# Optimization experiments

Measured on AMD Instinct MI355X. Metric: run time of the kernel, lower is better.

Reference implementation:

```python
import jax, jax.numpy as jnp
import numpy as np

LN_EPS = 1e-5
K = 3  # pointops.interpolation uses 3-NN

def _ln(x, g, b):
    mu = jnp.mean(x, axis=-1, keepdims=True)
    var = jnp.mean((x - mu) ** 2, axis=-1, keepdims=True)
    return (x - mu) * jax.lax.rsqrt(var + LN_EPS) * g + b

def setup_inputs() -> dict:
    key = jax.random.key(0)
    ks = jax.random.split(key, 8)
    B, n, m = 4, 4096, 16384        # coarse pts / fine pts per batch segment
    Cin, Cout = 384, 192
    feats = jax.random.normal(ks[0], (B * n, Cin), jnp.float32)
    xyz = jax.random.uniform(ks[1], (B * n, 3), jnp.float32)
    support_xyz = jax.random.uniform(ks[2], (B * m, 3), jnp.float32)
    support_feats = jax.random.normal(ks[3], (B * m, Cout), jnp.float32)
    offset = ((jnp.arange(B) + 1) * n).astype(jnp.int32)
    support_offset = ((jnp.arange(B) + 1) * m).astype(jnp.int32)
    # linear1: LayerNorm(Cout) -> Linear(Cout, Cout); linear2: LayerNorm(Cin) -> Linear(Cin, Cout)
    ln1_g = jnp.ones((Cout,), jnp.float32); ln1_b = jnp.zeros((Cout,), jnp.float32)
    w1 = jax.random.normal(ks[4], (Cout, Cout), jnp.float32) / np.sqrt(Cout)
    b1 = jnp.zeros((Cout,), jnp.float32)
    ln2_g = jnp.ones((Cin,), jnp.float32); ln2_b = jnp.zeros((Cin,), jnp.float32)
    w2 = jax.random.normal(ks[5], (Cin, Cout), jnp.float32) / np.sqrt(Cin)
    b2 = jnp.zeros((Cout,), jnp.float32)
    return {"feats": feats, "xyz": xyz, "support_xyz": support_xyz,
            "support_feats": support_feats, "offset": offset,
            "support_offset": support_offset, "ln1_g": ln1_g, "ln1_b": ln1_b,
            "w1": w1, "b1": b1, "ln2_g": ln2_g, "ln2_b": ln2_b, "w2": w2, "b2": b2}

def _interp_one(args):
    # src_xyz [n,3], dst_xyz [m,3], src_feat [n,C] -> [m,C]
    src_xyz, dst_xyz, src_feat = args
    d2 = jnp.sum((dst_xyz[:, None, :] - src_xyz[None, :, :]) ** 2, axis=-1)  # [m,n]
    neg_d2, idx = jax.lax.top_k(-d2, K)                                      # 3 nearest
    dist = jnp.sqrt(jnp.maximum(-neg_d2, 0.0))
    recip = 1.0 / (dist + 1e-8)
    w = recip / jnp.sum(recip, axis=-1, keepdims=True)                       # [m,K]
    return jnp.einsum('mk,mkc->mc', w, src_feat[idx])

def reference(feats, xyz, support_xyz, support_feats, offset, support_offset,
              ln1_g, ln1_b, w1, b1, ln2_g, ln2_b, w2, b2):
    B = offset.shape[0]
    n = feats.shape[0] // B
    m = support_feats.shape[0] // B
    # branch 2: LN+Linear on coarse feats, then 3-NN inverse-distance interpolation to fine points
    h = _ln(feats, ln2_g, ln2_b) @ w2 + b2                                   # [B*n, Cout]
    interp = jax.lax.map(_interp_one, (xyz.reshape(B, n, 3),
                                       support_xyz.reshape(B, m, 3),
                                       h.reshape(B, n, -1)))                 # [B,m,Cout]
    interp = interp.reshape(B * m, -1)
    # branch 1: LN+Linear skip on fine support features, fused add
    out = _ln(support_feats, ln1_g, ln1_b) @ w1 + b1 + interp
    return (out, support_xyz, support_offset)
```

## Files before the change

### kernel.cpp

```cpp
#include <hip/hip_runtime.h>
#include <cstddef>
#include <cstdint>

constexpr int B_SEG   = 4;
constexpr int N_C     = 4096;
constexpr int M_F     = 16384;
constexpr int CIN     = 384;
constexpr int COUT    = 192;
constexpr int MT      = B_SEG * N_C;
constexpr int MF      = B_SEG * M_F;
constexpr float LN_EPS = 1e-5f;

constexpr int GRES    = 16;
constexpr int NCELL   = GRES * GRES * GRES;

typedef __bf16 bf16x8 __attribute__((ext_vector_type(8)));
typedef __bf16 bf16x4 __attribute__((ext_vector_type(4)));
typedef float  f32x4  __attribute__((ext_vector_type(4)));

__global__ __launch_bounds__(256) void k0_prep(
    const float* __restrict__ w2, const float* __restrict__ w1,
    __bf16* __restrict__ wt2, __bf16* __restrict__ wt1)
{
  int e = blockIdx.x * 256 + threadIdx.x;
  if (e < CIN * COUT) {
    int k = e / COUT, n = e % COUT;
    wt2[(size_t)n * CIN + k] = (__bf16)w2[e];
  }
  e -= CIN * COUT;
  if (e >= 0 && e < COUT * COUT) {
    int k = e / COUT, n = e % COUT;
    wt1[(size_t)n * COUT + k] = (__bf16)w1[e];
  }
}

__global__ __launch_bounds__(256) void k1_ln_gemm(
    const float* __restrict__ feats, const float* __restrict__ ln_g,
    const float* __restrict__ ln_b, const __bf16* __restrict__ wt2,
    const float* __restrict__ b2, float* __restrict__ h)
{
  __shared__ __align__(16) __bf16 As[64][CIN + 8];
  const int tid = threadIdx.x;
  const int blk = blockIdx.x;

  {
    const int r = tid >> 2, q = tid & 3;
    const float* frow = feats + (size_t)(blk * 64 + r) * CIN;
    float4 v[24];
    float sum = 0.f, sumsq = 0.f;
#pragma unroll
    for (int i = 0; i < 24; ++i) {
      float4 t = *(const float4*)(frow + (q + 4 * i) * 4);
      v[i] = t;
      sum   += (t.x + t.y) + (t.z + t.w);
      sumsq += (t.x * t.x + t.y * t.y) + (t.z * t.z + t.w * t.w);
    }
    sum   += __shfl_xor(sum, 1);  sumsq += __shfl_xor(sumsq, 1);
    sum   += __shfl_xor(sum, 2);  sumsq += __shfl_xor(sumsq, 2);
    float mean = sum * (1.f / CIN);
    float var  = sumsq * (1.f / CIN) - mean * mean;
    if (var < 0.f) var = 0.f;
    float rs = rsqrtf(var + LN_EPS);
#pragma unroll
    for (int i = 0; i < 24; ++i) {
      float4 g4 = *(const float4*)(ln_g + (q + 4 * i) * 4);
      float4 b4 = *(const float4*)(ln_b + (q + 4 * i) * 4);
      bf16x4 o;
      o[0] = (__bf16)((v[i].x - mean) * rs * g4.x + b4.x);
      o[1] = (__bf16)((v[i].y - mean) * rs * g4.y + b4.y);
      o[2] = (__bf16)((v[i].z - mean) * rs * g4.z + b4.z);
      o[3] = (__bf16)((v[i].w - mean) * rs * g4.w + b4.w);
      *(bf16x4*)&As[r][(q + 4 * i) * 4] = o;
    }
  }
  __syncthreads();

  const int w = tid >> 6, lane = tid & 63, m = lane & 15, half = lane >> 4;
  f32x4 acc[12];
#pragma unroll
  for (int t = 0; t < 12; ++t) acc[t] = (f32x4){0.f, 0.f, 0.f, 0.f};

  const __bf16* Arow = &As[16 * w + m][half * 8];
  const __bf16* Bbase = wt2 + (size_t)m * CIN + half * 8;
#pragma unroll
  for (int ch = 0; ch < 12; ++ch) {
    bf16x8 a = *(const bf16x8*)(Arow + ch * 32);
#pragma unroll
    for (int t = 0; t < 12; ++t) {
      bf16x8 b = *(const bf16x8*)(Bbase + (size_t)(16 * t) * CIN + ch * 32);
      acc[t] = __builtin_amdgcn_mfma_f32_16x16x32_bf16(a, b, acc[t], 0, 0, 0);
    }
  }

  const int r0 = blk * 64 + 16 * w + half * 4;
#pragma unroll
  for (int t = 0; t < 12; ++t) {
    float bv = b2[16 * t + m];
#pragma unroll
    for (int reg = 0; reg < 4; ++reg)
      h[(size_t)(r0 + reg) * COUT + 16 * t + m] = acc[t][reg] + bv;
  }
}

__device__ __forceinline__ float dist2_rn(float px, float py, float pz,
                                          float sx, float sy, float sz)
{
  float dx = __fsub_rn(px, sx);
  float dy = __fsub_rn(py, sy);
  float dz = __fsub_rn(pz, sz);
  return __fadd_rn(__fadd_rn(__fmul_rn(dx, dx), __fmul_rn(dy, dy)),
                   __fmul_rn(dz, dz));
}

__device__ __forceinline__ void merge3(
    unsigned long long& a0, unsigned long long& a1, unsigned long long& a2,
    unsigned long long b0, unsigned long long b1, unsigned long long b2)
{
  bool t = a0 <= b0;
  unsigned long long r0 = t ? a0 : b0;
  unsigned long long A0 = t ? a1 : a0;
  unsigned long long A1 = t ? a2 : a1;
  unsigned long long B0 = t ? b0 : b1;
  unsigned long long B1 = t ? b1 : b2;
  t = A0 <= B0;
  unsigned long long r1 = t ? A0 : B0;
  unsigned long long C0 = t ? A1 : A0;
  unsigned long long D0 = t ? B0 : B1;
  unsigned long long r2 = C0 <= D0 ? C0 : D0;
  a0 = r0; a1 = r1; a2 = r2;
}

__device__ __forceinline__ void quad_merge(
    unsigned long long bk0, unsigned long long bk1, unsigned long long bk2,
    unsigned long long& m0, unsigned long long& m1, unsigned long long& m2)
{
  m0 = bk0; m1 = bk1; m2 = bk2;
  merge3(m0, m1, m2, __shfl_xor(bk0, 1), __shfl_xor(bk1, 1), __shfl_xor(bk2, 1));
  merge3(m0, m1, m2, __shfl_xor(m0, 2), __shfl_xor(m1, 2), __shfl_xor(m2, 2));
}

__global__ __launch_bounds__(256) void kgrid(
    const float* __restrict__ xyz,
    float4* __restrict__ pts_g, uint32_t* __restrict__ starts_g)
{
  __shared__ uint32_t cnt[NCELL];
  __shared__ uint32_t bsum[256];
  const int t = threadIdx.x;
  const int b = blockIdx.x;
  const float* src = xyz + (size_t)b * N_C * 3;

#pragma unroll
  for (int i = 0; i < NCELL / 256; ++i) cnt[t + 256 * i] = 0u;
  __syncthreads();

  int   cl[16];
  float xr[16], yr[16], zr[16];
#pragma unroll
  for (int i = 0; i < 16; ++i) {
    int p = i * 256 + t;
    float x = src[3 * p + 0], y = src[3 * p + 1], z = src[3 * p + 2];
    xr[i] = x; yr[i] = y; zr[i] = z;
    int ix = min(GRES - 1, max(0, (int)(x * (float)GRES)));
    int iy = min(GRES - 1, max(0, (int)(y * (float)GRES)));
    int iz = min(GRES - 1, max(0, (int)(z * (float)GRES)));
    int c = (ix << 8) | (iy << 4) | iz;
    cl[i] = c;
    atomicAdd(&cnt[c], 1u);
  }
  __syncthreads();

  uint32_t loc[16], s = 0;
#pragma unroll
  for (int j = 0; j < 16; ++j) { loc[j] = cnt[t * 16 + j]; s += loc[j]; }
  bsum[t] = s;
  __syncthreads();
  for (int off = 1; off < 256; off <<= 1) {
    uint32_t v = (t >= off) ? bsum[t - off] : 0u;
    __syncthreads();
    bsum[t] += v;
    __syncthreads();
  }
  uint32_t run = bsum[t] - s;
#pragma unroll
  for (int j = 0; j < 16; ++j) { cnt[t * 16 + j] = run; run += loc[j]; }
  __syncthreads();

#pragma unroll
  for (int i = 0; i < NCELL / 256; ++i)
    starts_g[(size_t)b * (NCELL + 1) + t + 256 * i] = cnt[t + 256 * i];
  if (t == 0) starts_g[(size_t)b * (NCELL + 1) + NCELL] = N_C;
  __syncthreads();

#pragma unroll
  for (int i = 0; i < 16; ++i) {
    int p = i * 256 + t;
    uint32_t pos = atomicAdd(&cnt[cl[i]], 1u);
    size_t o = (size_t)b * N_C + pos;
    pts_g[o] = make_float4(xr[i], yr[i], zr[i], __uint_as_float((uint32_t)p));
  }
}

__global__ __launch_bounds__(256) void kknn(
    const float* __restrict__ sxyz,
    const float4* __restrict__ pts_g, const uint32_t* __restrict__ starts_g,
    int* __restrict__ knn_i, float* __restrict__ knn_w)
{
  __shared__ uint32_t starts[NCELL + 1];
  const int tid = threadIdx.x;
  const int blk = blockIdx.x;
  const int b   = blk >> 8;

#pragma unroll
  for (int i = 0; i < 17; ++i) {
    int k = tid + 256 * i;
    if (k < NCELL + 1) starts[k] = starts_g[(size_t)b * (NCELL + 1) + k];
  }

  const float4* pb = pts_g + (size_t)b * N_C;
  const int sub = tid & 3;
  const int dst = blk * 64 + (tid >> 2);
  const float px = sxyz[(size_t)dst * 3 + 0];
  const float py = sxyz[(size_t)dst * 3 + 1];
  const float pz = sxyz[(size_t)dst * 3 + 2];
  const int cx = min(GRES - 1, max(0, (int)(px * (float)GRES)));
  const int cy = min(GRES - 1, max(0, (int)(py * (float)GRES)));
  const int cz = min(GRES - 1, max(0, (int)(pz * (float)GRES)));
  __syncthreads();

  unsigned long long bk0 = ~0ull, bk1 = ~0ull, bk2 = ~0ull;

  for (int xx = cx - 1; xx <= cx + 1; ++xx) {
    if ((unsigned)xx > (unsigned)(GRES - 1)) continue;
    for (int yy = cy - 1; yy <= cy + 1; ++yy) {
      if ((unsigned)yy > (unsigned)(GRES - 1)) continue;
      for (int zz = cz - 1; zz <= cz + 1; ++zz) {
        if ((unsigned)zz > (unsigned)(GRES - 1)) continue;
        int c = (xx << 8) | (yy << 4) | zz;
        for (uint32_t i = starts[c] + sub, e = starts[c + 1]; i < e; i += 4) {
          float4 p4 = pb[i];
          float d2 = dist2_rn(px, py, pz, p4.x, p4.y, p4.z);
          unsigned long long key =
              ((unsigned long long)__float_as_uint(d2) << 32) |
              (unsigned long long)__float_as_uint(p4.w);
          bool i0 = key < bk0, i1 = key < bk1, i2 = key < bk2;
          bk2 = i1 ? bk1 : (i2 ? key : bk2);
          bk1 = i0 ? bk0 : (i1 ? key : bk1);
          bk0 = i0 ? key : bk0;
        }
      }
    }
  }

  unsigned long long m0, m1, m2;
  quad_merge(bk0, bk1, bk2, m0, m1, m2);

  const float H = 1.0f / (float)GRES;
  float t2f = __uint_as_float((uint32_t)(m2 >> 32));
  if (!(t2f < H * H * 0.999999f)) {
    for (int R = 2; R <= GRES - 1; ++R) {
      int x0 = max(cx - R, 0), x1 = min(cx + R, GRES - 1);
      int y0 = max(cy - R, 0), y1 = min(cy + R, GRES - 1);
      int z0 = max(cz - R, 0), z1 = min(cz + R, GRES - 1);
      for (int xx = x0; xx <= x1; ++xx) {
        int ax = abs(xx - cx);
        for (int yy = y0; yy <= y1; ++yy) {
          int ay = abs(yy - cy);
          for (int zz = z0; zz <= z1; ++zz) {
            int ch = max(ax, max(ay, abs(zz - cz)));
            if (ch != R) continue;
            int c = (xx << 8) | (yy << 4) | zz;
            for (uint32_t i = starts[c] + sub, e = starts[c + 1]; i < e; i += 4) {
              float4 p4 = pb[i];
              float d2 = dist2_rn(px, py, pz, p4.x, p4.y, p4.z);
              unsigned long long key =
                  ((unsigned long long)__float_as_uint(d2) << 32) |
                  (unsigned long long)__float_as_uint(p4.w);
              bool i0 = key < bk0, i1 = key < bk1, i2 = key < bk2;
              bk2 = i1 ? bk1 : (i2 ? key : bk2);
              bk1 = i0 ? bk0 : (i1 ? key : bk1);
              bk0 = i0 ? key : bk0;
            }
          }
        }
      }
      quad_merge(bk0, bk1, bk2, m0, m1, m2);
      t2f = __uint_as_float((uint32_t)(m2 >> 32));
      float thr = (float)R * H;
      if (t2f < thr * thr * 0.999999f) break;
    }
  }

  if (sub == 0) {
    float d0  = sqrtf(__uint_as_float((uint32_t)(m0 >> 32)));
    float d1  = sqrtf(__uint_as_float((uint32_t)(m1 >> 32)));
    float d2s = sqrtf(__uint_as_float((uint32_t)(m2 >> 32)));
    float r0 = 1.f / (d0 + 1e-8f);
    float r1 = 1.f / (d1 + 1e-8f);
    float r2 = 1.f / (d2s + 1e-8f);
    float inv = 1.f / (r0 + r1 + r2);
    const int jb = b * N_C;
    knn_i[(size_t)dst * 3 + 0] = jb + (int)(m0 & 0xffffffffull);
    knn_i[(size_t)dst * 3 + 1] = jb + (int)(m1 & 0xffffffffull);
    knn_i[(size_t)dst * 3 + 2] = jb + (int)(m2 & 0xffffffffull);
    knn_w[(size_t)dst * 3 + 0] = r0 * inv;
    knn_w[(size_t)dst * 3 + 1] = r1 * inv;
    knn_w[(size_t)dst * 3 + 2] = r2 * inv;
  }
}

__global__ __launch_bounds__(256) void k3_ln_gemm_interp(
    const float* __restrict__ sfeats, const float* __restrict__ ln_g,
    const float* __restrict__ ln_b, const __bf16* __restrict__ wt1,
    const float* __restrict__ b1, const float* __restrict__ h,
    const int* __restrict__ knn_i, const float* __restrict__ knn_w,
    float* __restrict__ out)
{
  __shared__ __align__(16) __bf16 sm[64][COUT + 8];
  const int tid = threadIdx.x;
  const int blk = blockIdx.x;

  {
    const int r = tid >> 2, q = tid & 3;
    const float* frow = sfeats + (size_t)(blk * 64 + r) * COUT;
    float4 v[12];
    float sum = 0.f, sumsq = 0.f;
#pragma unroll
    for (int i = 0; i < 12; ++i) {
      float4 t = *(const float4*)(frow + (q + 4 * i) * 4);
      v[i] = t;
      sum   += (t.x + t.y) + (t.z + t.w);
      sumsq += (t.x * t.x + t.y * t.y) + (t.z * t.z + t.w * t.w);
    }
    sum   += __shfl_xor(sum, 1);  sumsq += __shfl_xor(sumsq, 1);
    sum   += __shfl_xor(sum, 2);  sumsq += __shfl_xor(sumsq, 2);
    float mean = sum * (1.f / COUT);
    float var  = sumsq * (1.f / COUT) - mean * mean;
    if (var < 0.f) var = 0.f;
    float rs = rsqrtf(var + LN_EPS);
#pragma unroll
    for (int i = 0; i < 12; ++i) {
      float4 g4 = *(const float4*)(ln_g + (q + 4 * i) * 4);
      float4 b4 = *(const float4*)(ln_b + (q + 4 * i) * 4);
      bf16x4 o;
      o[0] = (__bf16)((v[i].x - mean) * rs * g4.x + b4.x);
      o[1] = (__bf16)((v[i].y - mean) * rs * g4.y + b4.y);
      o[2] = (__bf16)((v[i].z - mean) * rs * g4.z + b4.z);
      o[3] = (__bf16)((v[i].w - mean) * rs * g4.w + b4.w);
      *(bf16x4*)&sm[r][(q + 4 * i) * 4] = o;
    }
  }
  __syncthreads();

  const int w = tid >> 6, lane = tid & 63, m = lane & 15, half = lane >> 4;
  f32x4 acc[12];
#pragma unroll
  for (int t = 0; t < 12; ++t) acc[t] = (f32x4){0.f, 0.f, 0.f, 0.f};

  const __bf16* Arow = &sm[16 * w + m][half * 8];
  const __bf16* Bbase = wt1 + (size_t)m * COUT + half * 8;
#pragma unroll
  for (int ch = 0; ch < 6; ++ch) {
    bf16x8 a = *(const bf16x8*)(Arow + ch * 32);
#pragma unroll
    for (int t = 0; t < 12; ++t) {
      bf16x8 b = *(const bf16x8*)(Bbase + (size_t)(16 * t) * COUT + ch * 32);
      acc[t] = __builtin_amdgcn_mfma_f32_16x16x32_bf16(a, b, acc[t], 0, 0, 0);
    }
  }

  float bv[12];
#pragma unroll
  for (int t = 0; t < 12; ++t) bv[t] = b1[16 * t + m];
  __syncthreads();
  {
    const int rr = 16 * w + half * 4;
#pragma unroll
    for (int t = 0; t < 12; ++t)
#pragma unroll
      for (int reg = 0; reg < 4; ++reg)
        sm[rr + reg][16 * t + m] = (__bf16)(acc[t][reg] + bv[t]);
  }
  __syncthreads();

  {
    const int r = tid >> 2, q = tid & 3;
    const int R = blk * 64 + r;
    int   i0 = knn_i[(size_t)R * 3 + 0];
    int   i1 = knn_i[(size_t)R * 3 + 1];
    int   i2 = knn_i[(size_t)R * 3 + 2];
    float w0 = knn_w[(size_t)R * 3 + 0];
    float w1v = knn_w[(size_t)R * 3 + 1];
    float w2v = knn_w[(size_t)R * 3 + 2];
    const float* h0 = h + (size_t)i0 * COUT;
    const float* h1 = h + (size_t)i1 * COUT;
    const float* h2 = h + (size_t)i2 * COUT;
    float* orow = out + (size_t)R * COUT;
#pragma unroll
    for (int i = 0; i < 12; ++i) {
      const int col = 16 * i + 4 * q;
      bf16x4 c4 = *(const bf16x4*)&sm[r][col];
      f32x4 g0 = *(const f32x4*)(h0 + col);
      f32x4 g1 = *(const f32x4*)(h1 + col);
      f32x4 g2 = *(const f32x4*)(h2 + col);
      f32x4 o;
      o[0] = (float)c4[0] + w0 * g0[0] + w1v * g1[0] + w2v * g2[0];
      o[1] = (float)c4[1] + w0 * g0[1] + w1v * g1[1] + w2v * g2[1];
      o[2] = (float)c4[2] + w0 * g0[2] + w1v * g1[2] + w2v * g2[2];
      o[3] = (float)c4[3] + w0 * g0[3] + w1v * g1[3] + w2v * g2[3];
      *(f32x4*)(orow + col) = o;
    }
  }
}

__global__ __launch_bounds__(256) void k4_tail(
    const float* __restrict__ sxyz, const int* __restrict__ soff,
    float* __restrict__ out_tail)
{
  const int t = blockIdx.x * 256 + threadIdx.x;
  if (t < MF * 3) out_tail[t] = sxyz[t];
  if (t < B_SEG) out_tail[MF * 3 + t] = (float)soff[t];
}

extern "C" void kernel_launch(void* const* d_in, const int* in_sizes, int n_in,
                              void* d_out, int out_size, void* d_ws, size_t ws_size,
                              hipStream_t stream)
{
  const float* feats  = (const float*)d_in[0];
  const float* xyz    = (const float*)d_in[1];
  const float* sxyz   = (const float*)d_in[2];
  const float* sfeats = (const float*)d_in[3];
  const int*   soff   = (const int*)d_in[5];
  const float* ln1_g  = (const float*)d_in[6];
  const float* ln1_b  = (const float*)d_in[7];
  const float* w1     = (const float*)d_in[8];
  const float* b1     = (const float*)d_in[9];
  const float* ln2_g  = (const float*)d_in[10];
  const float* ln2_b  = (const float*)d_in[11];
  const float* w2     = (const float*)d_in[12];
  const float* b2     = (const float*)d_in[13];
  float* out = (float*)d_out;

  float*    h       = (float*)d_ws;
  int*      knn_i   = (int*)(h + (size_t)MT * COUT);
  float*    knn_w   = (float*)(knn_i + (size_t)MF * 3);
  float4*   pts_g   = (float4*)(knn_w + (size_t)MF * 3);
  uint32_t* starts_g= (uint32_t*)(pts_g + (size_t)B_SEG * N_C);
  __bf16*   wt2     = (__bf16*)(starts_g + (size_t)B_SEG * (NCELL + 1));
  __bf16*   wt1     = wt2 + (size_t)COUT * CIN;

  k0_prep<<<(CIN * COUT + COUT * COUT) / 256, 256, 0, stream>>>(w2, w1, wt2, wt1);
  kgrid<<<B_SEG, 256, 0, stream>>>(xyz, pts_g, starts_g);
  k1_ln_gemm<<<MT / 64, 256, 0, stream>>>(feats, ln2_g, ln2_b, wt2, b2, h);
  kknn<<<(MF * 4) / 256, 256, 0, stream>>>(sxyz, pts_g, starts_g, knn_i, knn_w);
  k3_ln_gemm_interp<<<MF / 64, 256, 0, stream>>>(sfeats, ln1_g, ln1_b, wt1, b1,
                                                 h, knn_i, knn_w, out);
  k4_tail<<<(MF * 3) / 256, 256, 0, stream>>>(sxyz, soff, out + (size_t)MF * COUT);
}
```

Measured before the change: 281.4 us.

## Merge contiguous z-cells in kNN scan and widen fused LN-GEMM-interp blocks

The kNN search now scans each (x,y) column of neighbouring grid cells as one contiguous point range, since z is the fastest cell index. The ring expansion scans the whole z-span of a column when it lies on the shell, and only the two end cells otherwise. This cuts per-cell loop overhead and divergence. Separately, the fused LN+GEMM+interpolation kernel now runs 512 threads per 64-row tile, with 8 threads per row and 8 waves splitting the output columns. The kNN index and weight loads are hoisted to the start of that kernel so their latency overlaps the LayerNorm work. This raises parallelism and memory-level overlap, at the cost of more register pressure per block and each A fragment being read by two waves.

```diff
diff --git a/kernel.cpp b/kernel.cpp
--- a/kernel.cpp
+++ b/kernel.cpp
@@ -139,6 +139,24 @@
   merge3(m0, m1, m2, __shfl_xor(m0, 2), __shfl_xor(m1, 2), __shfl_xor(m2, 2));
 }
 
+__device__ __forceinline__ void scan_range(
+    const float4* __restrict__ pb, uint32_t i0, uint32_t i1, int sub,
+    float px, float py, float pz,
+    unsigned long long& bk0, unsigned long long& bk1, unsigned long long& bk2)
+{
+  for (uint32_t i = i0 + sub; i < i1; i += 4) {
+    float4 p4 = pb[i];
+    float d2 = dist2_rn(px, py, pz, p4.x, p4.y, p4.z);
+    unsigned long long key =
+        ((unsigned long long)__float_as_uint(d2) << 32) |
+        (unsigned long long)__float_as_uint(p4.w);
+    bool c0 = key < bk0, c1 = key < bk1, c2 = key < bk2;
+    bk2 = c1 ? bk1 : (c2 ? key : bk2);
+    bk1 = c0 ? bk0 : (c1 ? key : bk1);
+    bk0 = c0 ? key : bk0;
+  }
+}
+
 __global__ __launch_bounds__(256) void kgrid(
     const float* __restrict__ xyz,
     float4* __restrict__ pts_g, uint32_t* __restrict__ starts_g)
@@ -229,26 +247,16 @@
 
   unsigned long long bk0 = ~0ull, bk1 = ~0ull, bk2 = ~0ull;
 
-  for (int xx = cx - 1; xx <= cx + 1; ++xx) {
-    if ((unsigned)xx > (unsigned)(GRES - 1)) continue;
-    for (int yy = cy - 1; yy <= cy + 1; ++yy) {
-      if ((unsigned)yy > (unsigned)(GRES - 1)) continue;
-      for (int zz = cz - 1; zz <= cz + 1; ++zz) {
-        if ((unsigned)zz > (unsigned)(GRES - 1)) continue;
-        int c = (xx << 8) | (yy << 4) | zz;
-        for (uint32_t i = starts[c] + sub, e = starts[c + 1]; i < e; i += 4) {
-          float4 p4 = pb[i];
-          float d2 = dist2_rn(px, py, pz, p4.x, p4.y, p4.z);
-          unsigned long long key =
-              ((unsigned long long)__float_as_uint(d2) << 32) |
-              (unsigned long long)__float_as_uint(p4.w);
-          bool i0 = key < bk0, i1 = key < bk1, i2 = key < bk2;
-          bk2 = i1 ? bk1 : (i2 ? key : bk2);
-          bk1 = i0 ? bk0 : (i1 ? key : bk1);
-          bk0 = i0 ? key : bk0;
-        }
+  {
+    int xlo = max(cx - 1, 0), xhi = min(cx + 1, GRES - 1);
+    int ylo = max(cy - 1, 0), yhi = min(cy + 1, GRES - 1);
+    int zlo = max(cz - 1, 0), zhi = min(cz + 1, GRES - 1);
+    for (int xx = xlo; xx <= xhi; ++xx)
+      for (int yy = ylo; yy <= yhi; ++yy) {
+        int base = (xx << 8) | (yy << 4);
+        scan_range(pb, starts[base + zlo], starts[base + zhi + 1], sub,
+                   px, py, pz, bk0, bk1, bk2);
       }
-    }
   }
 
   unsigned long long m0, m1, m2;
@@ -265,20 +273,20 @@
         int ax = abs(xx - cx);
         for (int yy = y0; yy <= y1; ++yy) {
           int ay = abs(yy - cy);
-          for (int zz = z0; zz <= z1; ++zz) {
-            int ch = max(ax, max(ay, abs(zz - cz)));
-            if (ch != R) continue;
-            int c = (xx << 8) | (yy << 4) | zz;
-            for (uint32_t i = starts[c] + sub, e = starts[c + 1]; i < e; i += 4) {
-              float4 p4 = pb[i];
-              float d2 = dist2_rn(px, py, pz, p4.x, p4.y, p4.z);
-              unsigned long long key =
-                  ((unsigned long long)__float_as_uint(d2) << 32) |
-                  (unsigned long long)__float_as_uint(p4.w);
-              bool i0 = key < bk0, i1 = key < bk1, i2 = key < bk2;
-              bk2 = i1 ? bk1 : (i2 ? key : bk2);
-              bk1 = i0 ? bk0 : (i1 ? key : bk1);
-              bk0 = i0 ? key : bk0;
+          int base = (xx << 8) | (yy << 4);
+          if (ax == R || ay == R) {
+            scan_range(pb, starts[base + z0], starts[base + z1 + 1], sub,
+                       px, py, pz, bk0, bk1, bk2);
+          } else {
+            if (cz - R >= 0) {
+              int c = base + cz - R;
+              scan_range(pb, starts[c], starts[c + 1], sub,
+                         px, py, pz, bk0, bk1, bk2);
+            }
+            if (cz + R <= GRES - 1) {
+              int c = base + cz + R;
+              scan_range(pb, starts[c], starts[c + 1], sub,
+                         px, py, pz, bk0, bk1, bk2);
             }
           }
         }
@@ -308,7 +316,7 @@
   }
 }
 
-__global__ __launch_bounds__(256) void k3_ln_gemm_interp(
+__global__ __launch_bounds__(512) void k3_ln_gemm_interp(
     const float* __restrict__ sfeats, const float* __restrict__ ln_g,
     const float* __restrict__ ln_b, const __bf16* __restrict__ wt1,
     const float* __restrict__ b1, const float* __restrict__ h,
@@ -318,86 +326,91 @@
   __shared__ __align__(16) __bf16 sm[64][COUT + 8];
   const int tid = threadIdx.x;
   const int blk = blockIdx.x;
+  const int r = tid >> 3, q = tid & 7;
+  const int R = blk * 64 + r;
+
+  const int   gi0 = knn_i[(size_t)R * 3 + 0];
+  const int   gi1 = knn_i[(size_t)R * 3 + 1];
+  const int   gi2 = knn_i[(size_t)R * 3 + 2];
+  const float w0  = knn_w[(size_t)R * 3 + 0];
+  const float w1v = knn_w[(size_t)R * 3 + 1];
+  const float w2v = knn_w[(size_t)R * 3 + 2];
+  const float* h0 = h + (size_t)gi0 * COUT;
+  const float* h1 = h + (size_t)gi1 * COUT;
+  const float* h2 = h + (size_t)gi2 * COUT;
 
   {
-    const int r = tid >> 2, q = tid & 3;
-    const float* frow = sfeats + (size_t)(blk * 64 + r) * COUT;
-    float4 v[12];
+    const float* frow = sfeats + (size_t)R * COUT;
+    float4 v[6];
     float sum = 0.f, sumsq = 0.f;
 #pragma unroll
-    for (int i = 0; i < 12; ++i) {
-      float4 t = *(const float4*)(frow + (q + 4 * i) * 4);
+    for (int i = 0; i < 6; ++i) {
+      float4 t = *(const float4*)(frow + (q + 8 * i) * 4);
       v[i] = t;
       sum   += (t.x + t.y) + (t.z + t.w);
       sumsq += (t.x * t.x + t.y * t.y) + (t.z * t.z + t.w * t.w);
     }
     sum   += __shfl_xor(sum, 1);  sumsq += __shfl_xor(sumsq, 1);
     sum   += __shfl_xor(sum, 2);  sumsq += __shfl_xor(sumsq, 2);
+    sum   += __shfl_xor(sum, 4);  sumsq += __shfl_xor(sumsq, 4);
     float mean = sum * (1.f / COUT);
     float var  = sumsq * (1.f / COUT) - mean * mean;
     if (var < 0.f) var = 0.f;
     float rs = rsqrtf(var + LN_EPS);
 #pragma unroll
-    for (int i = 0; i < 12; ++i) {
-      float4 g4 = *(const float4*)(ln_g + (q + 4 * i) * 4);
-      float4 b4 = *(const float4*)(ln_b + (q + 4 * i) * 4);
+    for (int i = 0; i < 6; ++i) {
+      float4 g4 = *(const float4*)(ln_g + (q + 8 * i) * 4);
+      float4 b4 = *(const float4*)(ln_b + (q + 8 * i) * 4);
       bf16x4 o;
       o[0] = (__bf16)((v[i].x - mean) * rs * g4.x + b4.x);
       o[1] = (__bf16)((v[i].y - mean) * rs * g4.y + b4.y);
       o[2] = (__bf16)((v[i].z - mean) * rs * g4.z + b4.z);
       o[3] = (__bf16)((v[i].w - mean) * rs * g4.w + b4.w);
-      *(bf16x4*)&sm[r][(q + 4 * i) * 4] = o;
+      *(bf16x4*)&sm[r][(q + 8 * i) * 4] = o;
     }
   }
   __syncthreads();
 
   const int w = tid >> 6, lane = tid & 63, m = lane & 15, half = lane >> 4;
-  f32x4 acc[12];
-#pragma unroll
-  for (int t = 0; t < 12; ++t) acc[t] = (f32x4){0.f, 0.f, 0.f, 0.f};
-
-  const __bf16* Arow = &sm[16 * w + m][half * 8];
+  const int wr = w >> 1, nc = w & 1;
+  f32x4 acc[6];
+#pragma unroll
+  for (int t = 0; t < 6; ++t) acc[t] = (f32x4){0.f, 0.f, 0.f, 0.f};
+
+  const __bf16* Arow = &sm[16 * wr + m][half * 8];
   const __bf16* Bbase = wt1 + (size_t)m * COUT + half * 8;
 #pragma unroll
   for (int ch = 0; ch < 6; ++ch) {
     bf16x8 a = *(const bf16x8*)(Arow + ch * 32);
 #pragma unroll
-    for (int t = 0; t < 12; ++t) {
-      bf16x8 b = *(const bf16x8*)(Bbase + (size_t)(16 * t) * COUT + ch * 32);
+    for (int t = 0; t < 6; ++t) {
+      const int ct = nc * 6 + t;
+      bf16x8 b = *(const bf16x8*)(Bbase + (size_t)(16 * ct) * COUT + ch * 32);
       acc[t] = __builtin_amdgcn_mfma_f32_16x16x32_bf16(a, b, acc[t], 0, 0, 0);
     }
   }
 
-  float bv[12];
-#pragma unroll
-  for (int t = 0; t < 12; ++t) bv[t] = b1[16 * t + m];
+  float bv[6];
+#pragma unroll
+  for (int t = 0; t < 6; ++t) bv[t] = b1[16 * (nc * 6 + t) + m];
   __syncthreads();
   {
-    const int rr = 16 * w + half * 4;
-#pragma unroll
-    for (int t = 0; t < 12; ++t)
+    const int rr = 16 * wr + half * 4;
+#pragma unroll
+    for (int t = 0; t < 6; ++t) {
+      const int col = 16 * (nc * 6 + t) + m;
 #pragma unroll
       for (int reg = 0; reg < 4; ++reg)
-        sm[rr + reg][16 * t + m] = (__bf16)(acc[t][reg] + bv[t]);
+        sm[rr + reg][col] = (__bf16)(acc[t][reg] + bv[t]);
+    }
   }
   __syncthreads();
 
   {
-    const int r = tid >> 2, q = tid & 3;
-    const int R = blk * 64 + r;
-    int   i0 = knn_i[(size_t)R * 3 + 0];
-    int   i1 = knn_i[(size_t)R * 3 + 1];
-    int   i2 = knn_i[(size_t)R * 3 + 2];
-    float w0 = knn_w[(size_t)R * 3 + 0];
-    float w1v = knn_w[(size_t)R * 3 + 1];
-    float w2v = knn_w[(size_t)R * 3 + 2];
-    const float* h0 = h + (size_t)i0 * COUT;
-    const float* h1 = h + (size_t)i1 * COUT;
-    const float* h2 = h + (size_t)i2 * COUT;
     float* orow = out + (size_t)R * COUT;
 #pragma unroll
-    for (int i = 0; i < 12; ++i) {
-      const int col = 16 * i + 4 * q;
+    for (int i = 0; i < 6; ++i) {
+      const int col = (q + 8 * i) * 4;
       bf16x4 c4 = *(const bf16x4*)&sm[r][col];
       f32x4 g0 = *(const f32x4*)(h0 + col);
       f32x4 g1 = *(const f32x4*)(h1 + col);
@@ -452,7 +465,7 @@
   kgrid<<<B_SEG, 256, 0, stream>>>(xyz, pts_g, starts_g);
   k1_ln_gemm<<<MT / 64, 256, 0, stream>>>(feats, ln2_g, ln2_b, wt2, b2, h);
   kknn<<<(MF * 4) / 256, 256, 0, stream>>>(sxyz, pts_g, starts_g, knn_i, knn_w);
-  k3_ln_gemm_interp<<<MF / 64, 256, 0, stream>>>(sfeats, ln1_g, ln1_b, wt1, b1,
+  k3_ln_gemm_interp<<<MF / 64, 512, 0, stream>>>(sfeats, ln1_g, ln1_b, wt1, b1,
                                                  h, knn_i, knn_w, out);
   k4_tail<<<(MF * 3) / 256, 256, 0, stream>>>(sxyz, soff, out + (size_t)MF * COUT);
 }
```

After: 243.5 us. -13.5%, faster.
